# Kernel tuning notes

Hardware: AMD Instinct MI355X
Metric: run time of the kernel (lower is better)

## Reference

```python
import jax, jax.numpy as jnp
import numpy as np

NUM_HEADS = 8
NEG_SLOPE = 0.2


def typed_linear(x, W, etype):
    # x: [E, din], W: [T, din, dout], etype: [E] int. Grouped (per-edge-type) linear,
    # computed as T dense GEMMs with a per-edge select (T is small and static).
    out = jnp.zeros((x.shape[0], W.shape[2]), x.dtype)
    for t in range(W.shape[0]):
        out = out + jnp.where((etype == t)[:, None], x @ W[t], jnp.zeros((), x.dtype))
    return out


def setup_inputs() -> dict:
    key = jax.random.key(0)
    ks = jax.random.split(key, 9)
    N, E, IN = 50000, 800000, 128
    H, D = NUM_HEADS, 16
    HD = H * D  # 128
    T = 8  # num edge types
    s = 0.05
    return {
        "x": jax.random.normal(ks[0], (N, IN), jnp.float32),
        "src": jax.random.randint(ks[1], (E,), 0, N),
        "dst": jax.random.randint(ks[2], (E,), 0, N),
        "etype": jax.random.randint(ks[3], (E,), 0, T),
        "W_w": jax.random.normal(ks[4], (T, IN, HD), jnp.float32) * s,
        "W_al": jax.random.normal(ks[5], (T, HD, HD), jnp.float32) * s,
        "W_ar": jax.random.normal(ks[6], (T, HD, HD), jnp.float32) * s,
        "W_res": jax.random.normal(ks[7], (IN, HD), jnp.float32) * s,
        "b_res": jnp.zeros((HD,), jnp.float32),
    }


def reference(x, src, dst, etype, W_w, W_al, W_ar, W_res, b_res):
    N = x.shape[0]
    HD = W_w.shape[2]
    H = NUM_HEADS
    D = HD // H

    m = x[src]                                   # copy_u gather: [E, in]
    feat = typed_linear(m, W_w, etype)           # [E, H*D]
    h = feat                                     # dropout p=0 (eval/deterministic)

    # per-head attention logits
    h_l = typed_linear(h, W_al, etype).reshape(-1, H, D).sum(-1)  # [E, H]
    h_r = typed_linear(h, W_ar, etype).reshape(-1, H, D).sum(-1)  # [E, H]
    att = jax.nn.leaky_relu(h_l + h_r, NEG_SLOPE)

    # edge_softmax: segment softmax over incoming edges of each dst node
    att_max = jax.ops.segment_max(att, dst, num_segments=N)       # [N, H]
    att_exp = jnp.exp(att - att_max[dst])
    denom = jax.ops.segment_sum(att_exp, dst, num_segments=N)
    att = att_exp / denom[dst]                                    # [E, H]

    # NOTE: in the original source, 'alpha' is computed and stored in edata but the
    # aggregation copies edata 'm' (== h), so alpha never reaches the output.
    alpha = jnp.einsum('ehd,eh->ed', h.reshape(-1, H, D), att)    # [E, D] (dead)
    del alpha

    # update_all(copy_e('m'), sum): scatter-sum of h into dst nodes
    emb = jax.ops.segment_sum(h, dst, num_segments=N)             # [N, H*D]

    out = emb + x @ W_res + b_res                                 # residual
    return jax.nn.elu(out)
```

## Files before the change

### kernel.cpp

```cpp
#include <hip/hip_runtime.h>
#include <hip/hip_bf16.h>


#define KW 1152
#define CAP 3072
#define CHUNK 2048

typedef __bf16 bf16x8 __attribute__((ext_vector_type(8)));
typedef float f32x4 __attribute__((ext_vector_type(4)));

__device__ __forceinline__ void gload_lds16(const void* g, void* l) {
  __builtin_amdgcn_global_load_lds(
      (const __attribute__((address_space(1))) unsigned int*)g,
      (__attribute__((address_space(3))) unsigned int*)l, 16, 0, 0);
}

__device__ __forceinline__ float uflo(unsigned u) { return __uint_as_float(u << 16); }
__device__ __forceinline__ float ufhi(unsigned u) { return __uint_as_float(u & 0xffff0000u); }

__global__ __launch_bounds__(512) void k_binA(
    const int* __restrict__ src, const int* __restrict__ dst,
    const int* __restrict__ et, int* __restrict__ gCount,
    int* __restrict__ bucketBuf, int E) {
  __shared__ int buf[CHUNK];
  __shared__ short bkt[CHUNK];
  __shared__ int hist[512], sc[512], ls[512], cur[512], gb[512];
  const int tid = threadIdx.x;
  const int base = blockIdx.x * CHUNK;
  const int cnt = min(CHUNK, E - base);

  hist[tid] = 0;
  __syncthreads();
  for (int j = tid; j < cnt; j += 512) atomicAdd(&hist[dst[base + j] >> 7], 1);
  __syncthreads();
  sc[tid] = hist[tid];
  __syncthreads();
  for (int off = 1; off < 512; off <<= 1) {
    int t = (tid >= off) ? sc[tid - off] : 0;
    __syncthreads();
    if (tid >= off) sc[tid] += t;
    __syncthreads();
  }
  ls[tid] = sc[tid] - hist[tid];
  cur[tid] = ls[tid];
  gb[tid] = (hist[tid] > 0) ? atomicAdd(&gCount[tid], hist[tid]) : 0;
  __syncthreads();
  for (int j = tid; j < cnt; j += 512) {
    int e = base + j;
    int d = dst[e];
    int b = d >> 7;
    int pos = atomicAdd(&cur[b], 1);
    buf[pos] = (src[e] << 10) | (et[e] << 7) | (d & 127);
    bkt[pos] = (short)b;
  }
  __syncthreads();
  for (int j = tid; j < cnt; j += 512) {
    int b = bkt[j];
    bucketBuf[b * CAP + gb[b] + (j - ls[b])] = buf[j];
  }
}

__global__ __launch_bounds__(512) void k_scanC(
    const int* __restrict__ gCount, int* __restrict__ coarseBase,
    int* __restrict__ rowstart, int N, int E) {
  __shared__ int sc[512], h[512];
  int tid = threadIdx.x;
  h[tid] = gCount[tid];
  sc[tid] = h[tid];
  __syncthreads();
  for (int off = 1; off < 512; off <<= 1) {
    int t = (tid >= off) ? sc[tid - off] : 0;
    __syncthreads();
    if (tid >= off) sc[tid] += t;
    __syncthreads();
  }
  coarseBase[tid] = sc[tid] - h[tid];
  if (tid == 0) rowstart[N] = E;
}

__global__ __launch_bounds__(512) void k_sortB(
    const int* __restrict__ bucketBuf, const int* __restrict__ gCount,
    const int* __restrict__ coarseBase, int* __restrict__ rowstart,
    int* __restrict__ packed, int N) {
  __shared__ int raw[CAP];
  __shared__ int srt[CAP];
  __shared__ int hist[128], sc[128], bs[128], cur[128];
  const int b = blockIdx.x;
  const int tid = threadIdx.x;
  const int cnt = min(gCount[b], CAP);
  const int base = coarseBase[b];

  if (tid < 128) hist[tid] = 0;
  __syncthreads();
  for (int j = tid; j < cnt; j += 512) {
    int p = bucketBuf[b * CAP + j];
    raw[j] = p;
    atomicAdd(&hist[p & 127], 1);
  }
  __syncthreads();
  if (tid < 128) sc[tid] = hist[tid];
  __syncthreads();
  for (int off = 1; off < 128; off <<= 1) {
    int t = (tid < 128 && tid >= off) ? sc[tid - off] : 0;
    __syncthreads();
    if (tid < 128 && tid >= off) sc[tid] += t;
    __syncthreads();
  }
  if (tid < 128) {
    bs[tid] = sc[tid] - hist[tid];
    cur[tid] = bs[tid];
    int node = b * 128 + tid;
    if (node < N) rowstart[node] = base + bs[tid];
  }
  __syncthreads();
  for (int j = tid; j < cnt; j += 512) {
    int p = raw[j];
    int pos = atomicAdd(&cur[p & 127], 1);
    srt[pos] = p;
  }
  __syncthreads();
  for (int j = tid; j < cnt; j += 512) {
    int p = srt[j];
    packed[base + j] = (p >> 10) * 288 + (((p >> 7) & 7) << 5);
  }
}

__global__ void k_xcast(const float* __restrict__ x, ushort4* __restrict__ xb4,
                        int n4, int npad4) {
  int i = blockIdx.x * 256 + threadIdx.x;
  if (i >= npad4) return;
  ushort4 o = {0, 0, 0, 0};
  if (i < n4) {
    f32x4 v = *(const f32x4*)(x + i * 4);
    __hip_bfloat16 h0 = __float2bfloat16(v[0]), h1 = __float2bfloat16(v[1]);
    __hip_bfloat16 h2 = __float2bfloat16(v[2]), h3 = __float2bfloat16(v[3]);
    o.x = *(unsigned short*)&h0; o.y = *(unsigned short*)&h1;
    o.z = *(unsigned short*)&h2; o.w = *(unsigned short*)&h3;
  }
  xb4[i] = o;
}

__global__ void k_wb(const float* __restrict__ Ww, const float* __restrict__ Wres,
                     __hip_bfloat16* __restrict__ Wb) {
  int o = blockIdx.x * 256 + threadIdx.x;
  if (o >= KW * 128) return;
  int nn = o >> 7, kk = o & 127;
  float v = (nn < 1024) ? Ww[(nn >> 7) * 16384 + kk * 128 + (nn & 127)]
                        : Wres[kk * 128 + (nn & 127)];
  Wb[o] = __float2bfloat16(v);
}

__global__ __launch_bounds__(512) void k_ygemm(
    const __hip_bfloat16* __restrict__ xb, const __hip_bfloat16* __restrict__ Wb,
    unsigned short* __restrict__ y) {
  __shared__ __align__(16) unsigned short As[128 * 128];
  __shared__ __align__(16) unsigned short Bs[128 * 128];
  const int tid = threadIdx.x;
  const int lane = tid & 63;
  const int wid = tid >> 6;
  const int wr = wid >> 2, wc = wid & 3;
  const long row0 = (long)blockIdx.x * 128;

  const char* xbb = (const char*)xb;
  const char* wbb = (const char*)Wb;
  char* asb = (char*)As;
  char* bsb = (char*)Bs;

#pragma unroll
  for (int i = 0; i < 4; ++i) {
    int c = i * 512 + tid;
    int r = c >> 4, colb = (c & 15) << 4;
    int srcb = colb ^ ((r & 7) << 4);
    gload_lds16(xbb + (row0 + r) * 256 + srcb, asb + r * 256 + colb);
  }

  for (int g = 0; g < 9; ++g) {
#pragma unroll
    for (int i = 0; i < 4; ++i) {
      int c = i * 512 + tid;
      int r = c >> 4, colb = (c & 15) << 4;
      int srcb = colb ^ ((r & 7) << 4);
      gload_lds16(wbb + (long)(g * 128 + r) * 256 + srcb, bsb + r * 256 + colb);
    }
    asm volatile("s_waitcnt vmcnt(0)" ::: "memory");
    __syncthreads();

    f32x4 acc[4][2] = {};
#pragma unroll
    for (int ks = 0; ks < 4; ++ks) {
      const int cb = ks * 64 + ((lane >> 4) << 4);
      bf16x8 af[4], bfr[2];
#pragma unroll
      for (int mi = 0; mi < 4; ++mi) {
        int row = wr * 64 + mi * 16 + (lane & 15);
        af[mi] = *(const bf16x8*)(asb + ((row * 256 + cb) ^ ((row & 7) << 4)));
      }
#pragma unroll
      for (int ni = 0; ni < 2; ++ni) {
        int rowb = wc * 32 + ni * 16 + (lane & 15);
        bfr[ni] = *(const bf16x8*)(bsb + ((rowb * 256 + cb) ^ ((rowb & 7) << 4)));
      }
#pragma unroll
      for (int mi = 0; mi < 4; ++mi)
#pragma unroll
        for (int ni = 0; ni < 2; ++ni)
          acc[mi][ni] = __builtin_amdgcn_mfma_f32_16x16x32_bf16(
              af[mi], bfr[ni], acc[mi][ni], 0, 0, 0);
    }

#pragma unroll
    for (int mi = 0; mi < 4; ++mi)
#pragma unroll
      for (int ni = 0; ni < 2; ++ni) {
        int col = g * 128 + wc * 32 + ni * 16 + (lane & 15);
        long rb = row0 + wr * 64 + mi * 16 + ((lane >> 4) << 2);
        f32x4 v = acc[mi][ni];
#pragma unroll
        for (int q = 0; q < 4; ++q) {
          __hip_bfloat16 h = __float2bfloat16(v[q]);
          y[(rb + q) * KW + col] = *(unsigned short*)&h;
        }
      }
    __syncthreads();
  }
}

__global__ __launch_bounds__(256) void k_scat(
    const uint2* __restrict__ y4, const int* __restrict__ rowstart,
    const int* __restrict__ packed, const float* __restrict__ bres,
    float* __restrict__ out, int N) {
  const int w = threadIdx.x >> 6, lane = threadIdx.x & 63;
  const int n = blockIdx.x * 4 + w;
  if (n >= N) return;
  const int half = lane >> 5;
  const int sub = lane & 31;
  f32x4 a = {0.f, 0.f, 0.f, 0.f};
  int e = rowstart[n];
  const int end = rowstart[n + 1];

  for (; e + 16 <= end; e += 16) {
    uint2 r[8];
#pragma unroll
    for (int k = 0; k < 8; ++k) {
      int p = packed[e + 2 * k + half];
      r[k] = y4[p + sub];
    }
    __builtin_amdgcn_sched_barrier(0);
#pragma unroll
    for (int k = 0; k < 8; ++k) {
      a[0] += uflo(r[k].x); a[1] += ufhi(r[k].x);
      a[2] += uflo(r[k].y); a[3] += ufhi(r[k].y);
    }
  }
  for (; e + 2 <= end; e += 2) {
    int p = packed[e + half];
    uint2 r = y4[p + sub];
    a[0] += uflo(r.x); a[1] += ufhi(r.x);
    a[2] += uflo(r.y); a[3] += ufhi(r.y);
  }
  if (e < end) {
    int p = packed[e];
    uint2 r = y4[p + sub];
    if (!half) {
      a[0] += uflo(r.x); a[1] += ufhi(r.x);
      a[2] += uflo(r.y); a[3] += ufhi(r.y);
    }
  }
#pragma unroll
  for (int i = 0; i < 4; ++i) a[i] += __shfl_xor(a[i], 32);

  uint2 rr = y4[n * 288 + 256 + sub];
  f32x4 b4 = *(const f32x4*)(bres + sub * 4);
  a[0] += uflo(rr.x) + b4[0]; a[1] += ufhi(rr.x) + b4[1];
  a[2] += uflo(rr.y) + b4[2]; a[3] += ufhi(rr.y) + b4[3];
  f32x4 o;
#pragma unroll
  for (int i = 0; i < 4; ++i) o[i] = a[i] > 0.f ? a[i] : (expf(a[i]) - 1.f);
  if (!half)
    __builtin_nontemporal_store(o, (f32x4*)(out + (long)n * 128 + sub * 4));
}

extern "C" void kernel_launch(void* const* d_in, const int* in_sizes, int n_in,
                              void* d_out, int out_size, void* d_ws, size_t ws_size,
                              hipStream_t stream) {
  const float* x = (const float*)d_in[0];
  const int* src = (const int*)d_in[1];
  const int* dst = (const int*)d_in[2];
  const int* et = (const int*)d_in[3];
  const float* Ww = (const float*)d_in[4];
  const float* Wres = (const float*)d_in[7];
  const float* bres = (const float*)d_in[8];
  float* out = (float*)d_out;

  const int N = in_sizes[0] / 128;
  const int E = in_sizes[1];
  const int padM = ((N + 127) / 128) * 128;
  const int COARSE = (N + 127) >> 7;

  char* ws = (char*)d_ws;
  size_t off = 0;
  auto take = [&](size_t b) {
    char* p = ws + off;
    off = (off + b + 255) & ~(size_t)255;
    return p;
  };
  __hip_bfloat16* y = (__hip_bfloat16*)take((size_t)padM * KW * 2);
  __hip_bfloat16* Wb = (__hip_bfloat16*)take((size_t)KW * 128 * 2);
  __hip_bfloat16* xb = (__hip_bfloat16*)take((size_t)padM * 128 * 2);
  int* rowstart = (int*)take((size_t)(N + 1) * 4);
  int* gCount = (int*)take(512 * 4);
  int* coarseBase = (int*)take(512 * 4);
  int* packed = (int*)take((size_t)E * 4);
  int* bucketBuf = (int*)y;

  hipMemsetAsync(gCount, 0, 512 * 4, stream);
  k_binA<<<(E + CHUNK - 1) / CHUNK, 512, 0, stream>>>(src, dst, et, gCount, bucketBuf, E);
  k_scanC<<<1, 512, 0, stream>>>(gCount, coarseBase, rowstart, N, E);
  k_sortB<<<COARSE, 512, 0, stream>>>(bucketBuf, gCount, coarseBase, rowstart, packed, N);
  k_wb<<<(KW * 128 + 255) / 256, 256, 0, stream>>>(Ww, Wres, Wb);
  const int n4 = N * 128 / 4, npad4 = padM * 128 / 4;
  k_xcast<<<(npad4 + 255) / 256, 256, 0, stream>>>(x, (ushort4*)xb, n4, npad4);
  k_ygemm<<<padM / 128, 512, 0, stream>>>(xb, Wb, (unsigned short*)y);
  k_scat<<<(N + 3) / 4, 256, 0, stream>>>((const uint2*)y, rowstart, packed, bres, out, N);
}
```

Measured before the change: 198.4 us.

## Widen scatter loads to 16 bytes and coarsen dst buckets to 256 nodes

The gather-sum kernel now has each wavefront process four edges at a time, with 16 lanes reading 16-byte bf16 chunks per edge instead of two edges with 32 lanes reading 8 bytes. Partial sums are combined with two cross-lane shuffles. The binning pipeline switches to 256-node coarse buckets with double the capacity, which halves the bucket count and the scan size and repacks the src/etype/dst bit fields. The packed offsets are rescaled for uint4 indexing. The intent is fewer, wider memory transactions and fewer sort blocks, at the cost of more LDS in the sort kernel and a src bit budget that shrinks by one bit.

```diff
diff --git a/kernel.cpp b/kernel.cpp
--- a/kernel.cpp
+++ b/kernel.cpp
@@ -3,7 +3,7 @@
 
 
 #define KW 1152
-#define CAP 3072
+#define CAP 6144
 #define CHUNK 2048
 
 typedef __bf16 bf16x8 __attribute__((ext_vector_type(8)));
@@ -23,52 +23,55 @@
     const int* __restrict__ et, int* __restrict__ gCount,
     int* __restrict__ bucketBuf, int E) {
   __shared__ int buf[CHUNK];
-  __shared__ short bkt[CHUNK];
-  __shared__ int hist[512], sc[512], ls[512], cur[512], gb[512];
+  __shared__ unsigned char bkt[CHUNK];
+  __shared__ int h[256], ls[256], cur[256], gb[256], sc[256];
   const int tid = threadIdx.x;
   const int base = blockIdx.x * CHUNK;
   const int cnt = min(CHUNK, E - base);
 
-  hist[tid] = 0;
-  __syncthreads();
-  for (int j = tid; j < cnt; j += 512) atomicAdd(&hist[dst[base + j] >> 7], 1);
-  __syncthreads();
-  sc[tid] = hist[tid];
-  __syncthreads();
-  for (int off = 1; off < 512; off <<= 1) {
-    int t = (tid >= off) ? sc[tid - off] : 0;
-    __syncthreads();
-    if (tid >= off) sc[tid] += t;
-    __syncthreads();
-  }
-  ls[tid] = sc[tid] - hist[tid];
-  cur[tid] = ls[tid];
-  gb[tid] = (hist[tid] > 0) ? atomicAdd(&gCount[tid], hist[tid]) : 0;
+  if (tid < 256) h[tid] = 0;
+  __syncthreads();
+  for (int j = tid; j < cnt; j += 512) atomicAdd(&h[dst[base + j] >> 8], 1);
+  __syncthreads();
+  if (tid < 256) sc[tid] = h[tid];
+  __syncthreads();
+  for (int off = 1; off < 256; off <<= 1) {
+    int t = (tid < 256 && tid >= off) ? sc[tid - off] : 0;
+    __syncthreads();
+    if (tid < 256 && tid >= off) sc[tid] += t;
+    __syncthreads();
+  }
+  if (tid < 256) {
+    ls[tid] = sc[tid] - h[tid];
+    cur[tid] = ls[tid];
+    gb[tid] = (h[tid] > 0) ? atomicAdd(&gCount[tid], h[tid]) : 0;
+  }
   __syncthreads();
   for (int j = tid; j < cnt; j += 512) {
     int e = base + j;
     int d = dst[e];
-    int b = d >> 7;
+    int b = d >> 8;
     int pos = atomicAdd(&cur[b], 1);
-    buf[pos] = (src[e] << 10) | (et[e] << 7) | (d & 127);
-    bkt[pos] = (short)b;
+    buf[pos] = (src[e] << 11) | (et[e] << 8) | (d & 255);
+    bkt[pos] = (unsigned char)b;
   }
   __syncthreads();
   for (int j = tid; j < cnt; j += 512) {
     int b = bkt[j];
-    bucketBuf[b * CAP + gb[b] + (j - ls[b])] = buf[j];
-  }
-}
-
-__global__ __launch_bounds__(512) void k_scanC(
+    int pos = gb[b] + (j - ls[b]);
+    if (pos < CAP) bucketBuf[b * CAP + pos] = buf[j];
+  }
+}
+
+__global__ __launch_bounds__(256) void k_scanC(
     const int* __restrict__ gCount, int* __restrict__ coarseBase,
     int* __restrict__ rowstart, int N, int E) {
-  __shared__ int sc[512], h[512];
+  __shared__ int sc[256], h[256];
   int tid = threadIdx.x;
   h[tid] = gCount[tid];
   sc[tid] = h[tid];
   __syncthreads();
-  for (int off = 1; off < 512; off <<= 1) {
+  for (int off = 1; off < 256; off <<= 1) {
     int t = (tid >= off) ? sc[tid - off] : 0;
     __syncthreads();
     if (tid >= off) sc[tid] += t;
@@ -84,44 +87,44 @@
     int* __restrict__ packed, int N) {
   __shared__ int raw[CAP];
   __shared__ int srt[CAP];
-  __shared__ int hist[128], sc[128], bs[128], cur[128];
+  __shared__ int h[256], sc[256], bs[256], cur[256];
   const int b = blockIdx.x;
   const int tid = threadIdx.x;
   const int cnt = min(gCount[b], CAP);
   const int base = coarseBase[b];
 
-  if (tid < 128) hist[tid] = 0;
+  if (tid < 256) h[tid] = 0;
   __syncthreads();
   for (int j = tid; j < cnt; j += 512) {
     int p = bucketBuf[b * CAP + j];
     raw[j] = p;
-    atomicAdd(&hist[p & 127], 1);
-  }
-  __syncthreads();
-  if (tid < 128) sc[tid] = hist[tid];
-  __syncthreads();
-  for (int off = 1; off < 128; off <<= 1) {
-    int t = (tid < 128 && tid >= off) ? sc[tid - off] : 0;
-    __syncthreads();
-    if (tid < 128 && tid >= off) sc[tid] += t;
-    __syncthreads();
-  }
-  if (tid < 128) {
-    bs[tid] = sc[tid] - hist[tid];
+    atomicAdd(&h[p & 255], 1);
+  }
+  __syncthreads();
+  if (tid < 256) sc[tid] = h[tid];
+  __syncthreads();
+  for (int off = 1; off < 256; off <<= 1) {
+    int t = (tid < 256 && tid >= off) ? sc[tid - off] : 0;
+    __syncthreads();
+    if (tid < 256 && tid >= off) sc[tid] += t;
+    __syncthreads();
+  }
+  if (tid < 256) {
+    bs[tid] = sc[tid] - h[tid];
     cur[tid] = bs[tid];
-    int node = b * 128 + tid;
+    int node = b * 256 + tid;
     if (node < N) rowstart[node] = base + bs[tid];
   }
   __syncthreads();
   for (int j = tid; j < cnt; j += 512) {
     int p = raw[j];
-    int pos = atomicAdd(&cur[p & 127], 1);
+    int pos = atomicAdd(&cur[p & 255], 1);
     srt[pos] = p;
   }
   __syncthreads();
   for (int j = tid; j < cnt; j += 512) {
     int p = srt[j];
-    packed[base + j] = (p >> 10) * 288 + (((p >> 7) & 7) << 5);
+    packed[base + j] = (p >> 11) * 144 + (((p >> 8) & 7) << 4);
   }
 }
 
@@ -226,58 +229,86 @@
 }
 
 __global__ __launch_bounds__(256) void k_scat(
-    const uint2* __restrict__ y4, const int* __restrict__ rowstart,
+    const uint4* __restrict__ y16, const int* __restrict__ rowstart,
     const int* __restrict__ packed, const float* __restrict__ bres,
     float* __restrict__ out, int N) {
   const int w = threadIdx.x >> 6, lane = threadIdx.x & 63;
   const int n = blockIdx.x * 4 + w;
   if (n >= N) return;
-  const int half = lane >> 5;
-  const int sub = lane & 31;
-  f32x4 a = {0.f, 0.f, 0.f, 0.f};
+  const int q = lane >> 4;
+  const int sub = lane & 15;
+  float a[8] = {0.f, 0.f, 0.f, 0.f, 0.f, 0.f, 0.f, 0.f};
   int e = rowstart[n];
   const int end = rowstart[n + 1];
 
-  for (; e + 16 <= end; e += 16) {
-    uint2 r[8];
-#pragma unroll
-    for (int k = 0; k < 8; ++k) {
-      int p = packed[e + 2 * k + half];
-      r[k] = y4[p + sub];
-    }
+  for (; e + 32 <= end; e += 32) {
+    int p[8];
+    uint4 r[8];
+#pragma unroll
+    for (int k = 0; k < 8; ++k) p[k] = packed[e + 4 * k + q];
+#pragma unroll
+    for (int k = 0; k < 8; ++k) r[k] = y16[p[k] + sub];
     __builtin_amdgcn_sched_barrier(0);
 #pragma unroll
     for (int k = 0; k < 8; ++k) {
       a[0] += uflo(r[k].x); a[1] += ufhi(r[k].x);
       a[2] += uflo(r[k].y); a[3] += ufhi(r[k].y);
-    }
-  }
-  for (; e + 2 <= end; e += 2) {
-    int p = packed[e + half];
-    uint2 r = y4[p + sub];
-    a[0] += uflo(r.x); a[1] += ufhi(r.x);
-    a[2] += uflo(r.y); a[3] += ufhi(r.y);
-  }
-  if (e < end) {
-    int p = packed[e];
-    uint2 r = y4[p + sub];
-    if (!half) {
+      a[4] += uflo(r[k].z); a[5] += ufhi(r[k].z);
+      a[6] += uflo(r[k].w); a[7] += ufhi(r[k].w);
+    }
+  }
+  for (; e + 16 <= end; e += 16) {
+    int p[4];
+    uint4 r[4];
+#pragma unroll
+    for (int k = 0; k < 4; ++k) p[k] = packed[e + 4 * k + q];
+#pragma unroll
+    for (int k = 0; k < 4; ++k) r[k] = y16[p[k] + sub];
+    __builtin_amdgcn_sched_barrier(0);
+#pragma unroll
+    for (int k = 0; k < 4; ++k) {
+      a[0] += uflo(r[k].x); a[1] += ufhi(r[k].x);
+      a[2] += uflo(r[k].y); a[3] += ufhi(r[k].y);
+      a[4] += uflo(r[k].z); a[5] += ufhi(r[k].z);
+      a[6] += uflo(r[k].w); a[7] += ufhi(r[k].w);
+    }
+  }
+  for (; e < end; e += 4) {
+    int idx = e + q;
+    bool v = idx < end;
+    int p = packed[v ? idx : end - 1];
+    uint4 r = y16[p + sub];
+    if (v) {
       a[0] += uflo(r.x); a[1] += ufhi(r.x);
       a[2] += uflo(r.y); a[3] += ufhi(r.y);
-    }
-  }
-#pragma unroll
-  for (int i = 0; i < 4; ++i) a[i] += __shfl_xor(a[i], 32);
-
-  uint2 rr = y4[n * 288 + 256 + sub];
-  f32x4 b4 = *(const f32x4*)(bres + sub * 4);
-  a[0] += uflo(rr.x) + b4[0]; a[1] += ufhi(rr.x) + b4[1];
-  a[2] += uflo(rr.y) + b4[2]; a[3] += ufhi(rr.y) + b4[3];
-  f32x4 o;
-#pragma unroll
-  for (int i = 0; i < 4; ++i) o[i] = a[i] > 0.f ? a[i] : (expf(a[i]) - 1.f);
-  if (!half)
-    __builtin_nontemporal_store(o, (f32x4*)(out + (long)n * 128 + sub * 4));
+      a[4] += uflo(r.z); a[5] += ufhi(r.z);
+      a[6] += uflo(r.w); a[7] += ufhi(r.w);
+    }
+  }
+#pragma unroll
+  for (int i = 0; i < 8; ++i) {
+    a[i] += __shfl_xor(a[i], 16);
+    a[i] += __shfl_xor(a[i], 32);
+  }
+  uint4 rr = y16[n * 144 + 128 + sub];
+  a[0] += uflo(rr.x); a[1] += ufhi(rr.x);
+  a[2] += uflo(rr.y); a[3] += ufhi(rr.y);
+  a[4] += uflo(rr.z); a[5] += ufhi(rr.z);
+  a[6] += uflo(rr.w); a[7] += ufhi(rr.w);
+  f32x4 b0 = *(const f32x4*)(bres + sub * 8);
+  f32x4 b1 = *(const f32x4*)(bres + sub * 8 + 4);
+  f32x4 o0, o1;
+#pragma unroll
+  for (int i = 0; i < 4; ++i) {
+    float t0 = a[i] + b0[i];
+    float t1 = a[i + 4] + b1[i];
+    o0[i] = t0 > 0.f ? t0 : (expf(t0) - 1.f);
+    o1[i] = t1 > 0.f ? t1 : (expf(t1) - 1.f);
+  }
+  if (lane < 16) {
+    __builtin_nontemporal_store(o0, (f32x4*)(out + (long)n * 128 + sub * 8));
+    __builtin_nontemporal_store(o1, (f32x4*)(out + (long)n * 128 + sub * 8 + 4));
+  }
 }
 
 extern "C" void kernel_launch(void* const* d_in, const int* in_sizes, int n_in,
@@ -295,7 +326,7 @@
   const int N = in_sizes[0] / 128;
   const int E = in_sizes[1];
   const int padM = ((N + 127) / 128) * 128;
-  const int COARSE = (N + 127) >> 7;
+  const int COARSE = (N + 255) >> 8;
 
   char* ws = (char*)d_ws;
   size_t off = 0;
@@ -308,18 +339,18 @@
   __hip_bfloat16* Wb = (__hip_bfloat16*)take((size_t)KW * 128 * 2);
   __hip_bfloat16* xb = (__hip_bfloat16*)take((size_t)padM * 128 * 2);
   int* rowstart = (int*)take((size_t)(N + 1) * 4);
-  int* gCount = (int*)take(512 * 4);
-  int* coarseBase = (int*)take(512 * 4);
+  int* gCount = (int*)take(256 * 4);
+  int* coarseBase = (int*)take(256 * 4);
   int* packed = (int*)take((size_t)E * 4);
   int* bucketBuf = (int*)y;
 
-  hipMemsetAsync(gCount, 0, 512 * 4, stream);
+  hipMemsetAsync(gCount, 0, 256 * 4, stream);
   k_binA<<<(E + CHUNK - 1) / CHUNK, 512, 0, stream>>>(src, dst, et, gCount, bucketBuf, E);
-  k_scanC<<<1, 512, 0, stream>>>(gCount, coarseBase, rowstart, N, E);
+  k_scanC<<<1, 256, 0, stream>>>(gCount, coarseBase, rowstart, N, E);
   k_sortB<<<COARSE, 512, 0, stream>>>(bucketBuf, gCount, coarseBase, rowstart, packed, N);
   k_wb<<<(KW * 128 + 255) / 256, 256, 0, stream>>>(Ww, Wres, Wb);
   const int n4 = N * 128 / 4, npad4 = padM * 128 / 4;
   k_xcast<<<(npad4 + 255) / 256, 256, 0, stream>>>(x, (ushort4*)xb, n4, npad4);
   k_ygemm<<<padM / 128, 512, 0, stream>>>(xb, Wb, (unsigned short*)y);
-  k_scat<<<(N + 3) / 4, 256, 0, stream>>>((const uint2*)y, rowstart, packed, bres, out, N);
-}
+  k_scat<<<(N + 3) / 4, 256, 0, stream>>>((const uint4*)y, rowstart, packed, bres, out, N);
+}
```

After: 201.1 us. Within noise of the previous version (+1.3%).
